# Kernel optimization log

Measured on AMD Instinct MI355X. Metric: run time of the kernel, lower is better.

## Reference

```python
import jax, jax.numpy as jnp
import numpy as np

N, G, P, E = 65536, 256, 256, 1048576   # nodes, graphs, nodes/graph, edges
AF, BF, D, H, L, CE, T = 92, 41, 64, 128, 3, 16, 4
EPS = 1e-5


def _lin(x, W, b):
    return x @ W + b


def setup_inputs() -> dict:
    key = jax.random.key(0)
    ks = jax.random.split(key, 32)
    f = jax.random.normal
    inp = {
        "x": f(ks[0], (N, AF), jnp.float32),
        "edge_attr": f(ks[1], (E, BF), jnp.float32),
        "charge": f(ks[2], (G,), jnp.float32),
        "charge_W": f(ks[3], (1, CE)) * 0.3,
        "charge_b": f(ks[4], (CE,)) * 0.1,
        "atom_W": f(ks[5], (AF + CE, D)) * (1.0 / np.sqrt(AF + CE)),
        "atom_b": f(ks[6], (D,)) * 0.1,
        "bond_W": f(ks[7], (BF, D)) * (1.0 / np.sqrt(BF)),
        "bond_b": f(ks[8], (D,)) * 0.1,
        "nu_W1": f(ks[9], (L, 2 * D, D)) * (1.0 / np.sqrt(2 * D)),
        "nu_b1": f(ks[10], (L, D)) * 0.1,
        "nu_W2": f(ks[11], (L, D, D)) * (1.0 / np.sqrt(D)),
        "nu_b2": f(ks[12], (L, D)) * 0.1,
        "eu_W1": f(ks[13], (L, 3 * D, D)) * (1.0 / np.sqrt(3 * D)),
        "eu_b1": f(ks[14], (L, D)) * 0.1,
        "eu_W2": f(ks[15], (L, D, D)) * (1.0 / np.sqrt(D)),
        "eu_b2": f(ks[16], (L, D)) * 0.1,
        "bn_gamma": jnp.ones((L, D), jnp.float32),
        "bn_beta": jnp.zeros((L, D), jnp.float32),
        "pred_W1": f(ks[17], (D, H)) * (1.0 / np.sqrt(D)),
        "pred_b1": f(ks[18], (H,)) * 0.1,
        "pred_W2": f(ks[19], (H, H)) * (1.0 / np.sqrt(H)),
        "pred_b2": f(ks[20], (H,)) * 0.1,
        "pred_W3": f(ks[21], (H, 1)) * (1.0 / np.sqrt(H)),
        "pred_b3": f(ks[22], (1,)) * 0.1,
        "edge_index": jax.random.randint(ks[23], (2, E), 0, N, jnp.int32),
        "batch": (jnp.arange(N, dtype=jnp.int32) // P),
        "target_site_indices": jax.random.randint(ks[24], (G, T), 0, P, jnp.int32),
    }
    return inp


def reference(x, edge_attr, charge, charge_W, charge_b, atom_W, atom_b, bond_W,
              bond_b, nu_W1, nu_b1, nu_W2, nu_b2, eu_W1, eu_b1, eu_W2, eu_b2,
              bn_gamma, bn_beta, pred_W1, pred_b1, pred_W2, pred_b2, pred_W3,
              pred_b3, edge_index, batch, target_site_indices):
    sp = jax.nn.softplus
    # early charge integration
    charge_feat = _lin(charge[:, None], charge_W, charge_b)        # [G, CE]
    h = _lin(jnp.concatenate([x, charge_feat[batch]], 1), atom_W, atom_b)  # [N, D]
    e = _lin(edge_attr, bond_W, bond_b)                            # [E, D]
    row, col = edge_index[0], edge_index[1]
    for i in range(L):
        hs, hd = h[row], h[col]                                    # gather per edge
        e = _lin(sp(_lin(jnp.concatenate([hs, hd, e], 1), eu_W1[i], eu_b1[i])),
                 eu_W2[i], eu_b2[i])                               # edge update
        m = _lin(sp(_lin(jnp.concatenate([hs, e], 1), nu_W1[i], nu_b1[i])),
                 nu_W2[i], nu_b2[i])                               # messages
        hn = jax.ops.segment_sum(m, col, num_segments=N)           # scatter_add
        mu = hn.mean(0)
        var = hn.var(0)                                            # biased, as torch BN train
        hn = (hn - mu) / jnp.sqrt(var + EPS) * bn_gamma[i] + bn_beta[i]
        h = sp(hn) + h
    # selective pooling over target sites (vectorized version of per-graph loop)
    counts = jax.ops.segment_sum(jnp.ones((N,), h.dtype), batch, num_segments=G)
    counts_i = counts.astype(jnp.int32)
    starts = (jnp.cumsum(counts_i) - counts_i)                     # [G] graph offsets
    valid = target_site_indices < counts_i[:, None]                # [G, T]
    gidx = starts[:, None] + jnp.where(valid, target_site_indices, 0)
    sel = h[gidx] * valid[:, :, None].astype(h.dtype)              # [G, T, D]
    nsel = valid.sum(1)
    sel_mean = sel.sum(1) / jnp.maximum(nsel, 1)[:, None].astype(h.dtype)
    gmean = jax.ops.segment_sum(h, batch, num_segments=G) / counts[:, None]
    graph_repr = jnp.where((nsel > 0)[:, None], sel_mean, gmean)   # [G, D]
    # predictor (dropout = identity in eval)
    z = sp(_lin(graph_repr, pred_W1, pred_b1))
    z = sp(_lin(z, pred_W2, pred_b2))
    out = _lin(z, pred_W3, pred_b3)
    return out.squeeze(-1)                                         # [G]
```

## Files before the change

### kernel.cpp

```cpp
#include <hip/hip_runtime.h>
#include <hip/hip_bf16.h>
#include <hip/hip_fp16.h>
#include <math.h>

#define N_NODES 65536
#define N_GRAPH 256
#define P_NODES 256
#define N_EDGES 1048576
#define AF 92
#define BF 41
#define DIM 64
#define HID 128
#define NLAYER 3
#define CE 16
#define TS 4
#define BN_EPS 1e-5f
#define EPW 32
#define PSTRIDE 33

typedef _Float16 half8 __attribute__((ext_vector_type(8)));
typedef _Float16 half4_t __attribute__((ext_vector_type(4)));
typedef float floatx4 __attribute__((ext_vector_type(4)));

__device__ __forceinline__ float softplus_f(float x) {
    return fmaxf(x, 0.0f) + __logf(1.0f + __expf(-fabsf(x)));
}

__global__ __launch_bounds__(64) void k_h0(
    const float* __restrict__ x, const float* __restrict__ charge,
    const float* __restrict__ chW, const float* __restrict__ chb,
    const float* __restrict__ atomW, const float* __restrict__ atomb,
    const int* __restrict__ batch, float* __restrict__ h,
    __half* __restrict__ h16)
{
    const int n = blockIdx.x * 64 + threadIdx.x;
    float acc[DIM];
#pragma unroll
    for (int j = 0; j < DIM; ++j) acc[j] = atomb[j];
    const float* xr = x + (size_t)n * AF;
    for (int k2 = 0; k2 < AF; k2 += 2) {
        float2 a = *(const float2*)(xr + k2);
        {
            const float* w = atomW + (size_t)k2 * DIM;
#pragma unroll
            for (int j = 0; j < DIM; ++j) acc[j] = fmaf(w[j], a.x, acc[j]);
        }
        {
            const float* w = atomW + (size_t)(k2 + 1) * DIM;
#pragma unroll
            for (int j = 0; j < DIM; ++j) acc[j] = fmaf(w[j], a.y, acc[j]);
        }
    }
    const float cg = charge[batch[n]];
#pragma unroll
    for (int k = 0; k < CE; ++k) {
        float av = fmaf(cg, chW[k], chb[k]);
        const float* w = atomW + (size_t)(AF + k) * DIM;
#pragma unroll
        for (int j = 0; j < DIM; ++j) acc[j] = fmaf(w[j], av, acc[j]);
    }
    float* hp = h + (size_t)n * DIM;
    _Float16* hq = (_Float16*)h16 + (size_t)n * DIM;
#pragma unroll
    for (int j = 0; j < DIM; j += 4)
        *(float4*)(hp + j) = make_float4(acc[j], acc[j+1], acc[j+2], acc[j+3]);
#pragma unroll
    for (int j = 0; j < DIM; j += 8) {
        half8 hv;
#pragma unroll
        for (int u = 0; u < 8; ++u) hv[u] = (_Float16)acc[j + u];
        *(half8*)(hq + j) = hv;
    }
}

__global__ __launch_bounds__(256) void k_hist(const int* __restrict__ ecol,
                                              int* __restrict__ cnt)
{
    int t = blockIdx.x * 256 + threadIdx.x;
    atomicAdd(&cnt[ecol[t]], 1);
}

__global__ __launch_bounds__(256) void k_blksum(const int* __restrict__ cnt,
                                                int* __restrict__ bs)
{
    __shared__ int red[256];
    red[threadIdx.x] = cnt[blockIdx.x * 256 + threadIdx.x];
    __syncthreads();
    for (int o = 128; o > 0; o >>= 1) {
        if (threadIdx.x < o) red[threadIdx.x] += red[threadIdx.x + o];
        __syncthreads();
    }
    if (threadIdx.x == 0) bs[blockIdx.x] = red[0];
}

__global__ __launch_bounds__(256) void k_scanb(const int* __restrict__ bs,
                                               int* __restrict__ bo)
{
    __shared__ int ps[256];
    const int t = threadIdx.x;
    int v = bs[t];
    ps[t] = v;
    __syncthreads();
    for (int off = 1; off < 256; off <<= 1) {
        int u = (t >= off) ? ps[t - off] : 0;
        __syncthreads();
        ps[t] += u;
        __syncthreads();
    }
    bo[t] = ps[t] - v;
}

__global__ __launch_bounds__(256) void k_scan3(const int* __restrict__ cnt,
                                               const int* __restrict__ bo,
                                               int* __restrict__ starts)
{
    __shared__ int ps[256];
    const int b = blockIdx.x, t = threadIdx.x;
    int v = cnt[b * 256 + t];
    ps[t] = v;
    __syncthreads();
    for (int off = 1; off < 256; off <<= 1) {
        int u = (t >= off) ? ps[t - off] : 0;
        __syncthreads();
        ps[t] += u;
        __syncthreads();
    }
    starts[b * 256 + t] = bo[b] + ps[t] - v;
    if (b == 255 && t == 255) starts[N_NODES] = bo[255] + ps[255];
}

__global__ __launch_bounds__(256) void k_scatter(const int* __restrict__ ecol,
                                                 int* __restrict__ cur,
                                                 int* __restrict__ perm,
                                                 int* __restrict__ ipos)
{
    int t = blockIdx.x * 256 + threadIdx.x;
    int pos = atomicAdd(&cur[ecol[t]], 1);
    perm[pos] = t;
    ipos[t] = pos;
}

__global__ __launch_bounds__(256) void k_wprep_all(
    const float* __restrict__ euW1, const float* __restrict__ euW2,
    const float* __restrict__ nuW1, const float* __restrict__ nuW2,
    __half* __restrict__ out)
{
    const int idx = blockIdx.x * 256 + threadIdx.x;
    const int layer = idx / 28672;
    int off = idx - layer * 28672;
    const float* W;
    if (off < 12288)        { W = euW1 + (size_t)layer * 192 * DIM; }
    else if (off < 16384)   { W = euW2 + (size_t)layer * DIM * DIM; off -= 12288; }
    else if (off < 24576)   { W = nuW1 + (size_t)layer * 128 * DIM; off -= 16384; }
    else                    { W = nuW2 + (size_t)layer * DIM * DIM; off -= 24576; }
    int j    = off & 7;
    int lane = (off >> 3) & 63;
    int f    = off >> 9;
    int ntile = f & 3;
    int kIter = f >> 2;
    int k = kIter * 32 + ((lane >> 4) & 3) * 8 + j;
    int n = ntile * 16 + (lane & 15);
    out[idx] = __float2half(W[k * 64 + n]);
}

__global__ __launch_bounds__(256) void k_wprep_bond(
    const float* __restrict__ bondW, __half* __restrict__ out)
{
    const int idx = blockIdx.x * 256 + threadIdx.x;
    int j    = idx & 7;
    int lane = (idx >> 3) & 63;
    int f    = idx >> 9;
    int ntile = f & 3;
    int kIter = f >> 2;
    int k = kIter * 32 + ((lane >> 4) & 3) * 8 + j;
    int n = ntile * 16 + (lane & 15);
    out[idx] = (k < BF) ? __float2half(bondW[k * 64 + n]) : __float2half(0.0f);
}

__global__ __launch_bounds__(64) void k_wfuse(
    const float* __restrict__ euW2, const float* __restrict__ nuW1,
    const float* __restrict__ eub2, const float* __restrict__ nub1,
    float* __restrict__ WfuF32, float* __restrict__ bfu)
{
    const int L = blockIdx.x, j = threadIdx.x;
    const float* W2  = euW2 + (size_t)L * DIM * DIM;
    const float* N1b = nuW1 + (size_t)L * 128 * DIM + 64 * DIM;
    float acc[64];
#pragma unroll
    for (int k = 0; k < 64; ++k) acc[k] = 0.f;
    for (int l = 0; l < 64; ++l) {
        float nv = N1b[l * 64 + j];
#pragma unroll
        for (int k = 0; k < 64; ++k) acc[k] = fmaf(W2[k * 64 + l], nv, acc[k]);
    }
    float* outW = WfuF32 + (size_t)L * 4096;
    for (int k = 0; k < 64; ++k) outW[k * 64 + j] = acc[k];
    float b = nub1[L * 64 + j];
    for (int l = 0; l < 64; ++l) b = fmaf(eub2[L * 64 + l], N1b[l * 64 + j], b);
    bfu[L * 64 + j] = b;
}

__global__ __launch_bounds__(256) void k_wprep_fuse(
    const float* __restrict__ WfuF32, __half* __restrict__ out)
{
    const int idx = blockIdx.x * 256 + threadIdx.x;
    const int layer = idx >> 12;
    int off = idx & 4095;
    int j    = off & 7;
    int lane = (off >> 3) & 63;
    int f    = off >> 9;
    int ntile = f & 3;
    int kIter = f >> 2;
    int k = kIter * 32 + ((lane >> 4) & 3) * 8 + j;
    int n = ntile * 16 + (lane & 15);
    out[idx] = __float2half(WfuF32[(size_t)layer * 4096 + k * 64 + n]);
}

__device__ __forceinline__ void init_acc(floatx4 acc[2][4],
                                         const float* __restrict__ b, int mrow)
{
#pragma unroll
    for (int n = 0; n < 4; ++n) {
        float bv = b[n * 16 + mrow];
        floatx4 f = {bv, bv, bv, bv};
        acc[0][n] = f;
        acc[1][n] = f;
    }
}

__device__ __forceinline__ void gemm_panel(floatx4 acc[2][4],
                                           const _Float16* __restrict__ P,
                                           const __half* __restrict__ Wf,
                                           int fragBase, int quad,
                                           int mrow, int lane)
{
    const _Float16* Wh = (const _Float16*)Wf;
#pragma unroll
    for (int ki = 0; ki < 2; ++ki) {
        const _Float16* pa = P + (size_t)(((ki * 4 + quad) * PSTRIDE + mrow) * 8);
        half8 a0 = *(const half8*)pa;
        half8 a1 = *(const half8*)(pa + 16 * 8);
#pragma unroll
        for (int n = 0; n < 4; ++n) {
            half8 b = *(const half8*)(Wh +
                ((size_t)(fragBase + ki * 4 + n) * 64 + lane) * 8);
            acc[0][n] = __builtin_amdgcn_mfma_f32_16x16x32_f16(a0, b, acc[0][n], 0, 0, 0);
            acc[1][n] = __builtin_amdgcn_mfma_f32_16x16x32_f16(a1, b, acc[1][n], 0, 0, 0);
        }
    }
}

__device__ __forceinline__ void cstore_panel(const floatx4 acc[2][4],
                                             _Float16* __restrict__ P,
                                             int quad, int mrow, bool sp)
{
#pragma unroll
    for (int t = 0; t < 2; ++t)
#pragma unroll
        for (int n = 0; n < 4; ++n)
#pragma unroll
            for (int r = 0; r < 4; ++r) {
                int edge = t * 16 + quad * 4 + r;
                int d = n * 16 + mrow;
                float v = acc[t][n][r];
                if (sp) v = softplus_f(v);
                P[((d >> 3) * PSTRIDE + edge) * 8 + (d & 7)] = (_Float16)v;
            }
}

__device__ __forceinline__ void rows_to_global(const _Float16* __restrict__ P,
                                               __half* __restrict__ dst,
                                               int e0, int lane)
{
#pragma unroll
    for (int i = 0; i < 4; ++i) {
        int idx = i * 64 + lane;
        int eL = idx >> 3;
        int c  = idx & 7;
        half8 v = *(const half8*)&P[(c * PSTRIDE + eL) * 8];
        *(half8*)((_Float16*)dst + (size_t)(e0 + eL) * 64 + c * 8) = v;
    }
}

__device__ __forceinline__ void store_m_native(const floatx4 acc[2][4],
        __half* __restrict__ m, int blk, int quad, int mrow)
{
    _Float16* base = (_Float16*)m + (size_t)blk * 2048;
#pragma unroll
    for (int t = 0; t < 2; ++t)
#pragma unroll
        for (int n = 0; n < 4; ++n) {
            half4_t hv;
            hv[0] = (_Float16)acc[t][n][0];
            hv[1] = (_Float16)acc[t][n][1];
            hv[2] = (_Float16)acc[t][n][2];
            hv[3] = (_Float16)acc[t][n][3];
            *(half4_t*)(base + ((((t * 4 + n) * 4 + quad) * 16 + mrow) * 4)) = hv;
        }
}

__device__ __forceinline__ void stage_h16(const __half* __restrict__ hrow,
                                          _Float16* __restrict__ P,
                                          int sEdge, int sSeg)
{
    const _Float16* hp = (const _Float16*)hrow + sSeg * 32;
#pragma unroll
    for (int i = 0; i < 4; ++i) {
        half8 hv = *(const half8*)(hp + i * 8);
        *(half8*)&P[((sSeg * 4 + i) * PSTRIDE + sEdge) * 8] = hv;
    }
}

__global__ __launch_bounds__(64, 4) void k_edge4(
    const __half* __restrict__ h16, __half* __restrict__ eT,
    const __half* __restrict__ Wf, const __half* __restrict__ Wfu,
    const float* __restrict__ eub1, const float* __restrict__ eub2,
    const float* __restrict__ bfu,  const float* __restrict__ nub2,
    const int* __restrict__ erow, const int* __restrict__ ecol,
    const int* __restrict__ perm,
    __half* __restrict__ m)
{
    __shared__ __align__(16) _Float16 P0[8 * PSTRIDE * 8];
    __shared__ __align__(16) _Float16 P1[8 * PSTRIDE * 8];
    const int lane = threadIdx.x;
    const int quad = lane >> 4;
    const int mrow = lane & 15;
    const int e0   = blockIdx.x * EPW;
    const int sEdge = lane >> 1;
    const int sSeg  = lane & 1;

    floatx4 acc[2][4], acc2[2][4];

    half8 epre[4];
    {
        const _Float16* ep = (const _Float16*)(eT + (size_t)(e0 + sEdge) * DIM) + sSeg * 32;
#pragma unroll
        for (int i = 0; i < 4; ++i) epre[i] = *(const half8*)(ep + i * 8);
    }

    const int ed = perm[e0 + sEdge];
    stage_h16(h16 + (size_t)erow[ed] * DIM, P0, sEdge, sSeg);
    stage_h16(h16 + (size_t)ecol[ed] * DIM, P1, sEdge, sSeg);
    __syncthreads();

    init_acc(acc, eub1, mrow);
    gemm_panel(acc, P0, Wf, 0, quad, mrow, lane);
    gemm_panel(acc, P1, Wf, 8, quad, mrow, lane);
    __syncthreads();
    {
#pragma unroll
        for (int i = 0; i < 4; ++i)
            *(half8*)&P1[((sSeg * 4 + i) * PSTRIDE + sEdge) * 8] = epre[i];
    }
    __syncthreads();
    gemm_panel(acc, P1, Wf, 16, quad, mrow, lane);
    __syncthreads();
    cstore_panel(acc, P1, quad, mrow, true);
    __syncthreads();

    init_acc(acc, bfu, mrow);
    gemm_panel(acc, P0, Wf, 32, quad, mrow, lane);
    gemm_panel(acc, P1, Wfu, 0, quad, mrow, lane);
    init_acc(acc2, eub2, mrow);
    gemm_panel(acc2, P1, Wf, 24, quad, mrow, lane);
    __syncthreads();
    cstore_panel(acc, P0, quad, mrow, true);
    __syncthreads();

    init_acc(acc, nub2, mrow);
    gemm_panel(acc, P0, Wf, 48, quad, mrow, lane);
    __syncthreads();
    cstore_panel(acc2, P1, quad, mrow, false);
    __syncthreads();
    rows_to_global(P1, eT, e0, lane);
    store_m_native(acc, m, blockIdx.x, quad, mrow);
}

__global__ __launch_bounds__(256) void k_agg(
    const __half* __restrict__ m, const int* __restrict__ starts,
    __half* __restrict__ hn)
{
    const int w = threadIdx.x >> 6;
    const int lane = threadIdx.x & 63;
    const int n = blockIdx.x * 4 + w;
    const int s = starts[n], e = starts[n + 1];
    const int nn = lane >> 4, mrow = lane & 15;
    float acc = 0.f;
    for (int g = s & ~3; g < e; g += 4) {
        int blk = g >> 5;
        int off = g & 31;
        int t = off >> 4, quad = (off >> 2) & 3;
        half4_t v = *(const half4_t*)((const _Float16*)m + (size_t)blk * 2048
                     + (((t * 4 + nn) * 4 + quad) * 16 + mrow) * 4);
        float f0 = (float)v[0], f1 = (float)v[1];
        float f2 = (float)v[2], f3 = (float)v[3];
        if (g >= s && g + 3 < e) {
            acc += (f0 + f1) + (f2 + f3);
        } else {
            if (g     >= s && g     < e) acc += f0;
            if (g + 1 >= s && g + 1 < e) acc += f1;
            if (g + 2 >= s && g + 2 < e) acc += f2;
            if (g + 3 >= s && g + 3 < e) acc += f3;
        }
    }
    hn[(size_t)n * DIM + lane] = (__half)acc;
}

__global__ __launch_bounds__(256) void k_bnstats(const __half* __restrict__ hn,
                                                 float* __restrict__ stats)
{
    const int j = threadIdx.x & 63;
    const int sub = threadIdx.x >> 6;
    const int r0 = blockIdx.x * 256;
    float s = 0.f, qq = 0.f;
    for (int i = 0; i < 64; ++i) {
        float v = (float)hn[(size_t)(r0 + i * 4 + sub) * DIM + j];
        s += v;
        qq = fmaf(v, v, qq);
    }
    __shared__ float ls[256], lq[256];
    ls[threadIdx.x] = s; lq[threadIdx.x] = qq;
    __syncthreads();
    if (threadIdx.x < 128) {
        ls[threadIdx.x] += ls[threadIdx.x + 128];
        lq[threadIdx.x] += lq[threadIdx.x + 128];
    }
    __syncthreads();
    if (threadIdx.x < 64) {
        atomicAdd(&stats[j],      ls[threadIdx.x] + ls[threadIdx.x + 64]);
        atomicAdd(&stats[64 + j], lq[threadIdx.x] + lq[threadIdx.x + 64]);
    }
}

__global__ __launch_bounds__(256) void k_hupd(
    const __half* __restrict__ hn, float* __restrict__ h,
    __half* __restrict__ h16,
    const float* __restrict__ stats, const float* __restrict__ gamma,
    const float* __restrict__ beta)
{
    const size_t idx = (size_t)blockIdx.x * 256 + threadIdx.x;
    const int j = (int)(idx & 63);
    const float inv_n = 1.0f / (float)N_NODES;
    float mu  = stats[j] * inv_n;
    float var = stats[64 + j] * inv_n - mu * mu;
    float sc  = gamma[j] * rsqrtf(var + BN_EPS);
    float v   = ((float)hn[idx] - mu) * sc + beta[j];
    float nh  = h[idx] + softplus_f(v);
    h[idx] = nh;
    h16[idx] = (__half)nh;
}

__device__ __forceinline__ void stage_e2(_Float16* __restrict__ P,
                                         int id2, float2 v)
{
    int idx = id2 * 2;
    int e = (idx * 51151) >> 21;
    int k = idx - e * 41;
    P[((k >> 3) * PSTRIDE + e) * 8 + (k & 7)] = (_Float16)v.x;
    idx++;
    e = (idx * 51151) >> 21;
    k = idx - e * 41;
    P[((k >> 3) * PSTRIDE + e) * 8 + (k & 7)] = (_Float16)v.y;
}

__global__ __launch_bounds__(64) void k_e0m(
    const float* __restrict__ eattr, const __half* __restrict__ Wb,
    const float* __restrict__ bondb, const int* __restrict__ ipos,
    __half* __restrict__ eT)
{
    __shared__ __align__(16) _Float16 P0[8 * PSTRIDE * 8];
    __shared__ int slot[32];
    const int lane = threadIdx.x;
    const int quad = lane >> 4;
    const int mrow = lane & 15;
    const int e0   = blockIdx.x * 32;

    if (lane < 32) slot[lane] = ipos[e0 + lane];

    {
        half8 z = {};
#pragma unroll
        for (int i = 0; i < 4; ++i) ((half8*)P0)[i * 64 + lane] = z;
        if (lane < 8) ((half8*)P0)[256 + lane] = z;
    }
    __syncthreads();

    const float* src = eattr + (size_t)e0 * BF;
#pragma unroll
    for (int i = 0; i < 10; ++i) {
        const int id2 = i * 64 + lane;
        float2 v = *(const float2*)(src + id2 * 2);
        stage_e2(P0, id2, v);
    }
    if (lane < 16) {
        const int id2 = 640 + lane;
        float2 v = *(const float2*)(src + id2 * 2);
        stage_e2(P0, id2, v);
    }
    __syncthreads();

    floatx4 acc[2][4];
    init_acc(acc, bondb, mrow);
    gemm_panel(acc, P0, Wb, 0, quad, mrow, lane);
    __syncthreads();
    cstore_panel(acc, P0, quad, mrow, false);
    __syncthreads();

#pragma unroll
    for (int i = 0; i < 4; ++i) {
        int idx = i * 64 + lane;
        int eL = idx >> 3;
        int c  = idx & 7;
        half8 v = *(const half8*)&P0[(c * PSTRIDE + eL) * 8];
        *(half8*)((_Float16*)eT + (size_t)slot[eL] * DIM + c * 8) = v;
    }
}

__global__ __launch_bounds__(64) void k_pool(const float* __restrict__ h,
                                             const int* __restrict__ tsi,
                                             float* __restrict__ gr)
{
    const int g = blockIdx.x, j = threadIdx.x;
    float s = 0.f;
#pragma unroll
    for (int t = 0; t < TS; ++t) {
        int p = tsi[g * TS + t];
        s += h[(size_t)(g * P_NODES + p) * DIM + j];
    }
    gr[g * DIM + j] = s * (1.0f / TS);
}

__global__ __launch_bounds__(128) void k_pred(const float* __restrict__ gr,
    const float* __restrict__ W1, const float* __restrict__ b1,
    const float* __restrict__ W2, const float* __restrict__ b2,
    const float* __restrict__ W3, const float* __restrict__ b3,
    float* __restrict__ out)
{
    const int g = blockIdx.x, j = threadIdx.x;
    __shared__ float zin[DIM], z1[HID], red[HID];
    if (j < DIM) zin[j] = gr[g * DIM + j];
    __syncthreads();
    float a = b1[j];
    for (int k = 0; k < DIM; ++k) a = fmaf(zin[k], W1[k * HID + j], a);
    z1[j] = softplus_f(a);
    __syncthreads();
    float a2 = b2[j];
    for (int k = 0; k < HID; ++k) a2 = fmaf(z1[k], W2[k * HID + j], a2);
    red[j] = softplus_f(a2) * W3[j];
    __syncthreads();
    for (int s = 64; s > 0; s >>= 1) {
        if (j < s) red[j] += red[j + s];
        __syncthreads();
    }
    if (j == 0) out[g] = red[0] + b3[0];
}

extern "C" void kernel_launch(void* const* d_in, const int* in_sizes, int n_in,
                              void* d_out, int out_size, void* d_ws, size_t ws_size,
                              hipStream_t stream)
{
    const float* x      = (const float*)d_in[0];
    const float* eattr  = (const float*)d_in[1];
    const float* charge = (const float*)d_in[2];
    const float* chW    = (const float*)d_in[3];
    const float* chb    = (const float*)d_in[4];
    const float* atomW  = (const float*)d_in[5];
    const float* atomb  = (const float*)d_in[6];
    const float* bondW  = (const float*)d_in[7];
    const float* bondb  = (const float*)d_in[8];
    const float* nuW1   = (const float*)d_in[9];
    const float* nub1   = (const float*)d_in[10];
    const float* nuW2   = (const float*)d_in[11];
    const float* nub2   = (const float*)d_in[12];
    const float* euW1   = (const float*)d_in[13];
    const float* eub1   = (const float*)d_in[14];
    const float* euW2   = (const float*)d_in[15];
    const float* eub2   = (const float*)d_in[16];
    const float* gamma  = (const float*)d_in[17];
    const float* beta   = (const float*)d_in[18];
    const float* pW1    = (const float*)d_in[19];
    const float* pb1    = (const float*)d_in[20];
    const float* pW2    = (const float*)d_in[21];
    const float* pb2    = (const float*)d_in[22];
    const float* pW3    = (const float*)d_in[23];
    const float* pb3    = (const float*)d_in[24];
    const int*   eidx   = (const int*)d_in[25];
    const int*   batch  = (const int*)d_in[26];
    const int*   tsi    = (const int*)d_in[27];
    const int* erow = eidx;
    const int* ecol = eidx + N_EDGES;

    char* ws = (char*)d_ws;
    float*  h      = (float*)(ws);
    __half* hn     = (__half*)(ws + ((size_t)16 << 20));
    int*    ipos   = (int*)  (ws + ((size_t)16 << 20));
    __half* h16    = (__half*)(ws + ((size_t)24 << 20));
    float*  stats  = (float*)(ws + ((size_t)32 << 20));
    float*  gr     = (float*)(ws + ((size_t)32 << 20) + (64 << 10));
    int*    bs     = (int*)  (ws + ((size_t)32 << 20) + (192 << 10));
    int*    bo     = (int*)  (ws + ((size_t)32 << 20) + (196 << 10));
    int*    counts = (int*)  (ws + ((size_t)33 << 20));
    int*    starts = (int*)  (ws + ((size_t)33 << 20) + (256 << 10));
    int*    cur    = (int*)  (ws + ((size_t)33 << 20) + (768 << 10));
    __half* Wfrag  = (__half*)(ws + ((size_t)34 << 20));
    __half* Wbond  = (__half*)(ws + ((size_t)34 << 20) + (256 << 10));
    __half* Wfu    = (__half*)(ws + ((size_t)34 << 20) + (320 << 10));
    float*  bfu    = (float*)(ws + ((size_t)34 << 20) + (384 << 10));
    float*  WfuF32 = (float*)(ws + ((size_t)34 << 20) + (448 << 10));
    int*    perm   = (int*)  (ws + ((size_t)35 << 20));
    __half* eT     = (__half*)(ws + ((size_t)40 << 20));
    __half* m      = (__half*)(ws + ((size_t)168 << 20));

    hipMemsetAsync(counts, 0, N_NODES * sizeof(int), stream);
    k_hist<<<N_EDGES / 256, 256, 0, stream>>>(ecol, counts);
    k_blksum<<<256, 256, 0, stream>>>(counts, bs);
    k_scanb<<<1, 256, 0, stream>>>(bs, bo);
    k_scan3<<<256, 256, 0, stream>>>(counts, bo, starts);
    hipMemcpyAsync(cur, starts, N_NODES * sizeof(int),
                   hipMemcpyDeviceToDevice, stream);
    k_scatter<<<N_EDGES / 256, 256, 0, stream>>>(ecol, cur, perm, ipos);

    k_wprep_all<<<(3 * 28672) / 256, 256, 0, stream>>>(euW1, euW2, nuW1, nuW2, Wfrag);
    k_wprep_bond<<<16, 256, 0, stream>>>(bondW, Wbond);
    k_wfuse<<<3, 64, 0, stream>>>(euW2, nuW1, eub2, nub1, WfuF32, bfu);
    k_wprep_fuse<<<48, 256, 0, stream>>>(WfuF32, Wfu);

    k_h0<<<N_NODES / 64, 64, 0, stream>>>(x, charge, chW, chb, atomW, atomb,
                                          batch, h, h16);
    k_e0m<<<N_EDGES / 32, 64, 0, stream>>>(eattr, Wbond, bondb, ipos, eT);

    const size_t LW = 28672;
    for (int i = 0; i < NLAYER; ++i) {
        hipMemsetAsync(stats, 0, 128 * sizeof(float), stream);
        k_edge4<<<N_EDGES / EPW, 64, 0, stream>>>(h16, eT, Wfrag + i * LW,
            Wfu + (size_t)i * 4096,
            eub1 + i * DIM, eub2 + i * DIM, bfu + i * DIM, nub2 + i * DIM,
            erow, ecol, perm, m);
        k_agg<<<N_NODES / 4, 256, 0, stream>>>(m, starts, hn);
        k_bnstats<<<N_NODES / 256, 256, 0, stream>>>(hn, stats);
        k_hupd<<<(N_NODES * DIM) / 256, 256, 0, stream>>>(hn, h, h16, stats,
            gamma + i * DIM, beta + i * DIM);
    }

    k_pool<<<N_GRAPH, 64, 0, stream>>>(h, tsi, gr);
    k_pred<<<N_GRAPH, HID, 0, stream>>>(gr, pW1, pb1, pW2, pb2, pW3, pb3, (float*)d_out);
}
```

Measured before the change: 1.278 ms.

## Rewrite edge kernel with register-resident 32x32x16 MFMA chain, no LDS staging

Replaces the LDS-staged 16x16 MFMA edge kernel with one that loads gathered node and edge rows straight into 32x32x16 MFMA operands. Intermediate activations are passed between chained GEMMs in registers using lane shuffles, and biases are folded in as an extra ones column of K. Weight prep is reorganised into a single fragment-layout kernel, and the aggregation kernel is adapted to the new message layout with wider loads and a shuffle reduction. The aim is to remove LDS round trips and barriers in the per-layer edge work. The cost is higher register pressure and some padded MFMA work for the bias K-slices.

```diff
diff --git a/kernel.cpp b/kernel.cpp
--- a/kernel.cpp
+++ b/kernel.cpp
@@ -15,15 +15,43 @@
 #define CE 16
 #define TS 4
 #define BN_EPS 1e-5f
-#define EPW 32
 #define PSTRIDE 33
 
 typedef _Float16 half8 __attribute__((ext_vector_type(8)));
-typedef _Float16 half4_t __attribute__((ext_vector_type(4)));
 typedef float floatx4 __attribute__((ext_vector_type(4)));
+typedef float floatx16 __attribute__((ext_vector_type(16)));
 
 __device__ __forceinline__ float softplus_f(float x) {
     return fmaxf(x, 0.0f) + __logf(1.0f + __expf(-fabsf(x)));
+}
+
+__device__ __forceinline__ int pkcvt(float a, float b) {
+    __half2 h = __floats2half2_rn(a, b);
+    int r; __builtin_memcpy(&r, &h, 4); return r;
+}
+
+__device__ __forceinline__ half8 mk8(int a, int b, int c, int d) {
+    union { half8 v; int i[4]; } u;
+    u.i[0] = a; u.i[1] = b; u.i[2] = c; u.i[3] = d;
+    return u.v;
+}
+
+__device__ __forceinline__ floatx16 mfma32(half8 a, half8 b, floatx16 c) {
+    return __builtin_amdgcn_mfma_f32_32x32x16_f16(a, b, c, 0, 0, 0);
+}
+
+__device__ __forceinline__ half8 chain_frag(const floatx16& t, int s_local, bool hi) {
+    const int rA = 8 * s_local;
+    const int rB = rA + 4;
+    int A0 = pkcvt(t[rA + 0], t[rA + 1]);
+    int A1 = pkcvt(t[rA + 2], t[rA + 3]);
+    int B0 = pkcvt(t[rB + 0], t[rB + 1]);
+    int B1 = pkcvt(t[rB + 2], t[rB + 3]);
+    int S0 = hi ? A0 : B0, S1 = hi ? A1 : B1;
+    int R0 = __shfl_xor(S0, 32), R1 = __shfl_xor(S1, 32);
+    int w0 = hi ? R0 : A0, w1 = hi ? R1 : A1;
+    int w2 = hi ? B0 : R0, w3 = hi ? B1 : R1;
+    return mk8(w0, w1, w2, w3);
 }
 
 __global__ __launch_bounds__(64) void k_h0(
@@ -138,29 +166,6 @@
     int pos = atomicAdd(&cur[ecol[t]], 1);
     perm[pos] = t;
     ipos[t] = pos;
-}
-
-__global__ __launch_bounds__(256) void k_wprep_all(
-    const float* __restrict__ euW1, const float* __restrict__ euW2,
-    const float* __restrict__ nuW1, const float* __restrict__ nuW2,
-    __half* __restrict__ out)
-{
-    const int idx = blockIdx.x * 256 + threadIdx.x;
-    const int layer = idx / 28672;
-    int off = idx - layer * 28672;
-    const float* W;
-    if (off < 12288)        { W = euW1 + (size_t)layer * 192 * DIM; }
-    else if (off < 16384)   { W = euW2 + (size_t)layer * DIM * DIM; off -= 12288; }
-    else if (off < 24576)   { W = nuW1 + (size_t)layer * 128 * DIM; off -= 16384; }
-    else                    { W = nuW2 + (size_t)layer * DIM * DIM; off -= 24576; }
-    int j    = off & 7;
-    int lane = (off >> 3) & 63;
-    int f    = off >> 9;
-    int ntile = f & 3;
-    int kIter = f >> 2;
-    int k = kIter * 32 + ((lane >> 4) & 3) * 8 + j;
-    int n = ntile * 16 + (lane & 15);
-    out[idx] = __float2half(W[k * 64 + n]);
 }
 
 __global__ __launch_bounds__(256) void k_wprep_bond(
@@ -200,20 +205,48 @@
     bfu[L * 64 + j] = b;
 }
 
-__global__ __launch_bounds__(256) void k_wprep_fuse(
-    const float* __restrict__ WfuF32, __half* __restrict__ out)
+__global__ __launch_bounds__(256) void k_wprepB(
+    const float* __restrict__ euW1, const float* __restrict__ eub1,
+    const float* __restrict__ euW2, const float* __restrict__ eub2,
+    const float* __restrict__ nuW1, const float* __restrict__ WfuF32,
+    const float* __restrict__ bfu,  const float* __restrict__ nuW2,
+    const float* __restrict__ nub2, __half* __restrict__ out)
 {
     const int idx = blockIdx.x * 256 + threadIdx.x;
-    const int layer = idx >> 12;
-    int off = idx & 4095;
-    int j    = off & 7;
-    int lane = (off >> 3) & 63;
-    int f    = off >> 9;
-    int ntile = f & 3;
-    int kIter = f >> 2;
-    int k = kIter * 32 + ((lane >> 4) & 3) * 8 + j;
-    int n = ntile * 16 + (lane & 15);
-    out[idx] = __float2half(WfuF32[(size_t)layer * 4096 + k * 64 + n]);
+    const int L = idx >> 15;
+    const int off = idx & 32767;
+    const int F = off >> 9;
+    const int l = (off >> 3) & 63;
+    const int j = off & 7;
+    const int k_oct = ((l >> 5) << 3) + j;
+    const int row = (l & 31);
+    float val;
+    if (F < 26) {
+        int mt = F / 13, ks = F - mt * 13;
+        int k = ks * 16 + k_oct, r = mt * 32 + row;
+        val = (k < 192) ? euW1[(size_t)L * 192 * DIM + k * 64 + r]
+            : (k == 192 ? eub1[L * 64 + r] : 0.f);
+    } else if (F < 36) {
+        int f = F - 26; int mt = f / 5, ks = f - mt * 5;
+        int k = ks * 16 + k_oct, r = mt * 32 + row;
+        val = (k < 64) ? euW2[(size_t)L * 4096 + k * 64 + r]
+            : (k == 64 ? eub2[L * 64 + r] : 0.f);
+    } else if (F < 44) {
+        int f = F - 36; int mt = f / 4, ks = f - mt * 4;
+        int k = ks * 16 + k_oct, r = mt * 32 + row;
+        val = nuW1[(size_t)L * 8192 + k * 64 + r];
+    } else if (F < 54) {
+        int f = F - 44; int mt = f / 5, ks = f - mt * 5;
+        int k = ks * 16 + k_oct, r = mt * 32 + row;
+        val = (k < 64) ? WfuF32[(size_t)L * 4096 + k * 64 + r]
+            : (k == 64 ? bfu[L * 64 + r] : 0.f);
+    } else {
+        int f = F - 54; int mt = f / 5, ks = f - mt * 5;
+        int k = ks * 16 + k_oct, r = mt * 32 + row;
+        val = (k < 64) ? nuW2[(size_t)L * 4096 + k * 64 + r]
+            : (k == 64 ? nub2[L * 64 + r] : 0.f);
+    }
+    out[idx] = __float2half(val);
 }
 
 __device__ __forceinline__ void init_acc(floatx4 acc[2][4],
@@ -268,112 +301,194 @@
             }
 }
 
-__device__ __forceinline__ void rows_to_global(const _Float16* __restrict__ P,
-                                               __half* __restrict__ dst,
-                                               int e0, int lane)
-{
+__device__ __forceinline__ void stage_e2(_Float16* __restrict__ P,
+                                         int id2, float2 v)
+{
+    int idx = id2 * 2;
+    int e = (idx * 51151) >> 21;
+    int k = idx - e * 41;
+    P[((k >> 3) * PSTRIDE + e) * 8 + (k & 7)] = (_Float16)v.x;
+    idx++;
+    e = (idx * 51151) >> 21;
+    k = idx - e * 41;
+    P[((k >> 3) * PSTRIDE + e) * 8 + (k & 7)] = (_Float16)v.y;
+}
+
+__global__ __launch_bounds__(64) void k_e0m(
+    const float* __restrict__ eattr, const __half* __restrict__ Wb,
+    const float* __restrict__ bondb, const int* __restrict__ ipos,
+    __half* __restrict__ eT)
+{
+    __shared__ __align__(16) _Float16 P0[8 * PSTRIDE * 8];
+    __shared__ int slot[32];
+    const int lane = threadIdx.x;
+    const int quad = lane >> 4;
+    const int mrow = lane & 15;
+    const int e0   = blockIdx.x * 32;
+
+    if (lane < 32) slot[lane] = ipos[e0 + lane];
+
+    {
+        half8 z = {};
+#pragma unroll
+        for (int i = 0; i < 4; ++i) ((half8*)P0)[i * 64 + lane] = z;
+        if (lane < 8) ((half8*)P0)[256 + lane] = z;
+    }
+    __syncthreads();
+
+    const float* src = eattr + (size_t)e0 * BF;
+#pragma unroll
+    for (int i = 0; i < 10; ++i) {
+        const int id2 = i * 64 + lane;
+        float2 v = *(const float2*)(src + id2 * 2);
+        stage_e2(P0, id2, v);
+    }
+    if (lane < 16) {
+        const int id2 = 640 + lane;
+        float2 v = *(const float2*)(src + id2 * 2);
+        stage_e2(P0, id2, v);
+    }
+    __syncthreads();
+
+    floatx4 acc[2][4];
+    init_acc(acc, bondb, mrow);
+    gemm_panel(acc, P0, Wb, 0, quad, mrow, lane);
+    __syncthreads();
+    cstore_panel(acc, P0, quad, mrow, false);
+    __syncthreads();
+
 #pragma unroll
     for (int i = 0; i < 4; ++i) {
         int idx = i * 64 + lane;
         int eL = idx >> 3;
         int c  = idx & 7;
-        half8 v = *(const half8*)&P[(c * PSTRIDE + eL) * 8];
-        *(half8*)((_Float16*)dst + (size_t)(e0 + eL) * 64 + c * 8) = v;
-    }
-}
-
-__device__ __forceinline__ void store_m_native(const floatx4 acc[2][4],
-        __half* __restrict__ m, int blk, int quad, int mrow)
-{
-    _Float16* base = (_Float16*)m + (size_t)blk * 2048;
-#pragma unroll
-    for (int t = 0; t < 2; ++t)
-#pragma unroll
-        for (int n = 0; n < 4; ++n) {
-            half4_t hv;
-            hv[0] = (_Float16)acc[t][n][0];
-            hv[1] = (_Float16)acc[t][n][1];
-            hv[2] = (_Float16)acc[t][n][2];
-            hv[3] = (_Float16)acc[t][n][3];
-            *(half4_t*)(base + ((((t * 4 + n) * 4 + quad) * 16 + mrow) * 4)) = hv;
+        half8 v = *(const half8*)&P0[(c * PSTRIDE + eL) * 8];
+        *(half8*)((_Float16*)eT + (size_t)slot[eL] * DIM + c * 8) = v;
+    }
+}
+
+__global__ __launch_bounds__(64) void k_edge5(
+    const __half* __restrict__ h16, __half* __restrict__ eT,
+    const __half* __restrict__ WB,
+    const int* __restrict__ erow, const int* __restrict__ ecol,
+    const int* __restrict__ perm, __half* __restrict__ m)
+{
+    const int lane = threadIdx.x;
+    const int e = lane & 31;
+    const bool hi = lane >= 32;
+    const int h = hi ? 1 : 0;
+    const int e0 = blockIdx.x * 32;
+    const int ed = perm[e0 + e];
+    const int rs = erow[ed], cs = ecol[ed];
+
+    const half8* WBv = (const half8*)WB;
+
+    half8 fs[4], fd[4], fe[4];
+    {
+        const _Float16* ps = (const _Float16*)h16 + (size_t)rs * DIM + h * 8;
+        const _Float16* pd = (const _Float16*)h16 + (size_t)cs * DIM + h * 8;
+        const _Float16* pe = (const _Float16*)eT  + (size_t)(e0 + e) * DIM + h * 8;
+#pragma unroll
+        for (int s = 0; s < 4; ++s) {
+            fs[s] = *(const half8*)(ps + 16 * s);
+            fd[s] = *(const half8*)(pd + 16 * s);
+            fe[s] = *(const half8*)(pe + 16 * s);
         }
-}
-
-__device__ __forceinline__ void stage_h16(const __half* __restrict__ hrow,
-                                          _Float16* __restrict__ P,
-                                          int sEdge, int sSeg)
-{
-    const _Float16* hp = (const _Float16*)hrow + sSeg * 32;
-#pragma unroll
-    for (int i = 0; i < 4; ++i) {
-        half8 hv = *(const half8*)(hp + i * 8);
-        *(half8*)&P[((sSeg * 4 + i) * PSTRIDE + sEdge) * 8] = hv;
-    }
-}
-
-__global__ __launch_bounds__(64, 4) void k_edge4(
-    const __half* __restrict__ h16, __half* __restrict__ eT,
-    const __half* __restrict__ Wf, const __half* __restrict__ Wfu,
-    const float* __restrict__ eub1, const float* __restrict__ eub2,
-    const float* __restrict__ bfu,  const float* __restrict__ nub2,
-    const int* __restrict__ erow, const int* __restrict__ ecol,
-    const int* __restrict__ perm,
-    __half* __restrict__ m)
-{
-    __shared__ __align__(16) _Float16 P0[8 * PSTRIDE * 8];
-    __shared__ __align__(16) _Float16 P1[8 * PSTRIDE * 8];
-    const int lane = threadIdx.x;
-    const int quad = lane >> 4;
-    const int mrow = lane & 15;
-    const int e0   = blockIdx.x * EPW;
-    const int sEdge = lane >> 1;
-    const int sSeg  = lane & 1;
-
-    floatx4 acc[2][4], acc2[2][4];
-
-    half8 epre[4];
+    }
+    half8 ones = {};
+    if (!hi) ones[0] = (_Float16)1.0f;
+
+    floatx16 t1a = {};
+    floatx16 t1b = {};
+#pragma unroll
+    for (int ks = 0; ks < 13; ++ks) {
+        half8 b;
+        if (ks < 4)       b = fs[ks & 3];
+        else if (ks < 8)  b = fd[(ks - 4) & 3];
+        else if (ks < 12) b = fe[(ks - 8) & 3];
+        else              b = ones;
+        t1a = mfma32(WBv[(0 * 13 + ks) * 64 + lane], b, t1a);
+        t1b = mfma32(WBv[(1 * 13 + ks) * 64 + lane], b, t1b);
+    }
+#pragma unroll
+    for (int i = 0; i < 16; ++i) {
+        t1a[i] = softplus_f(t1a[i]);
+        t1b[i] = softplus_f(t1b[i]);
+    }
+    half8 bf1[4];
+    bf1[0] = chain_frag(t1a, 0, hi);
+    bf1[1] = chain_frag(t1a, 1, hi);
+    bf1[2] = chain_frag(t1b, 0, hi);
+    bf1[3] = chain_frag(t1b, 1, hi);
+
+    floatx16 ea = {};
+    floatx16 eb = {};
+#pragma unroll
+    for (int ks = 0; ks < 5; ++ks) {
+        half8 b;
+        if (ks < 4) b = bf1[ks & 3]; else b = ones;
+        ea = mfma32(WBv[(26 + 0 * 5 + ks) * 64 + lane], b, ea);
+        eb = mfma32(WBv[(26 + 1 * 5 + ks) * 64 + lane], b, eb);
+    }
     {
-        const _Float16* ep = (const _Float16*)(eT + (size_t)(e0 + sEdge) * DIM) + sSeg * 32;
-#pragma unroll
-        for (int i = 0; i < 4; ++i) epre[i] = *(const half8*)(ep + i * 8);
-    }
-
-    const int ed = perm[e0 + sEdge];
-    stage_h16(h16 + (size_t)erow[ed] * DIM, P0, sEdge, sSeg);
-    stage_h16(h16 + (size_t)ecol[ed] * DIM, P1, sEdge, sSeg);
-    __syncthreads();
-
-    init_acc(acc, eub1, mrow);
-    gemm_panel(acc, P0, Wf, 0, quad, mrow, lane);
-    gemm_panel(acc, P1, Wf, 8, quad, mrow, lane);
-    __syncthreads();
+        _Float16* dst = (_Float16*)eT + (size_t)(e0 + e) * DIM + 4 * h;
+#pragma unroll
+        for (int rg = 0; rg < 4; ++rg) {
+            int2 v; v.x = pkcvt(ea[4*rg+0], ea[4*rg+1]);
+            v.y = pkcvt(ea[4*rg+2], ea[4*rg+3]);
+            *(int2*)(dst + 8 * rg) = v;
+            int2 w; w.x = pkcvt(eb[4*rg+0], eb[4*rg+1]);
+            w.y = pkcvt(eb[4*rg+2], eb[4*rg+3]);
+            *(int2*)(dst + 32 + 8 * rg) = w;
+        }
+    }
+
+    floatx16 t2a = {};
+    floatx16 t2b = {};
+#pragma unroll
+    for (int ks = 0; ks < 4; ++ks) {
+        t2a = mfma32(WBv[(36 + 0 * 4 + ks) * 64 + lane], fs[ks], t2a);
+        t2b = mfma32(WBv[(36 + 1 * 4 + ks) * 64 + lane], fs[ks], t2b);
+    }
+#pragma unroll
+    for (int ks = 0; ks < 5; ++ks) {
+        half8 b;
+        if (ks < 4) b = bf1[ks & 3]; else b = ones;
+        t2a = mfma32(WBv[(44 + 0 * 5 + ks) * 64 + lane], b, t2a);
+        t2b = mfma32(WBv[(44 + 1 * 5 + ks) * 64 + lane], b, t2b);
+    }
+#pragma unroll
+    for (int i = 0; i < 16; ++i) {
+        t2a[i] = softplus_f(t2a[i]);
+        t2b[i] = softplus_f(t2b[i]);
+    }
+    half8 bf2[4];
+    bf2[0] = chain_frag(t2a, 0, hi);
+    bf2[1] = chain_frag(t2a, 1, hi);
+    bf2[2] = chain_frag(t2b, 0, hi);
+    bf2[3] = chain_frag(t2b, 1, hi);
+
+    floatx16 ma = {};
+    floatx16 mb = {};
+#pragma unroll
+    for (int ks = 0; ks < 5; ++ks) {
+        half8 b;
+        if (ks < 4) b = bf2[ks & 3]; else b = ones;
+        ma = mfma32(WBv[(54 + 0 * 5 + ks) * 64 + lane], b, ma);
+        mb = mfma32(WBv[(54 + 1 * 5 + ks) * 64 + lane], b, mb);
+    }
     {
-#pragma unroll
-        for (int i = 0; i < 4; ++i)
-            *(half8*)&P1[((sSeg * 4 + i) * PSTRIDE + sEdge) * 8] = epre[i];
-    }
-    __syncthreads();
-    gemm_panel(acc, P1, Wf, 16, quad, mrow, lane);
-    __syncthreads();
-    cstore_panel(acc, P1, quad, mrow, true);
-    __syncthreads();
-
-    init_acc(acc, bfu, mrow);
-    gemm_panel(acc, P0, Wf, 32, quad, mrow, lane);
-    gemm_panel(acc, P1, Wfu, 0, quad, mrow, lane);
-    init_acc(acc2, eub2, mrow);
-    gemm_panel(acc2, P1, Wf, 24, quad, mrow, lane);
-    __syncthreads();
-    cstore_panel(acc, P0, quad, mrow, true);
-    __syncthreads();
-
-    init_acc(acc, nub2, mrow);
-    gemm_panel(acc, P0, Wf, 48, quad, mrow, lane);
-    __syncthreads();
-    cstore_panel(acc2, P1, quad, mrow, false);
-    __syncthreads();
-    rows_to_global(P1, eT, e0, lane);
-    store_m_native(acc, m, blockIdx.x, quad, mrow);
+        _Float16* base = (_Float16*)m + (size_t)blockIdx.x * 2048;
+#pragma unroll
+        for (int rg = 0; rg < 4; ++rg) {
+            int2 v; v.x = pkcvt(ma[4*rg+0], ma[4*rg+1]);
+            v.y = pkcvt(ma[4*rg+2], ma[4*rg+3]);
+            *(int2*)(base + (rg * 64 + lane) * 4) = v;
+            int2 w; w.x = pkcvt(mb[4*rg+0], mb[4*rg+1]);
+            w.y = pkcvt(mb[4*rg+2], mb[4*rg+3]);
+            *(int2*)(base + ((4 + rg) * 64 + lane) * 4) = w;
+        }
+    }
 }
 
 __global__ __launch_bounds__(256) void k_agg(
@@ -384,26 +499,28 @@
     const int lane = threadIdx.x & 63;
     const int n = blockIdx.x * 4 + w;
     const int s = starts[n], e = starts[n + 1];
-    const int nn = lane >> 4, mrow = lane & 15;
-    float acc = 0.f;
-    for (int g = s & ~3; g < e; g += 4) {
-        int blk = g >> 5;
-        int off = g & 31;
-        int t = off >> 4, quad = (off >> 2) & 3;
-        half4_t v = *(const half4_t*)((const _Float16*)m + (size_t)blk * 2048
-                     + (((t * 4 + nn) * 4 + quad) * 16 + mrow) * 4);
-        float f0 = (float)v[0], f1 = (float)v[1];
-        float f2 = (float)v[2], f3 = (float)v[3];
-        if (g >= s && g + 3 < e) {
-            acc += (f0 + f1) + (f2 + f3);
-        } else {
-            if (g     >= s && g     < e) acc += f0;
-            if (g + 1 >= s && g + 1 < e) acc += f1;
-            if (g + 2 >= s && g + 2 < e) acc += f2;
-            if (g + 3 >= s && g + 3 < e) acc += f3;
-        }
-    }
-    hn[(size_t)n * DIM + lane] = (__half)acc;
+    const int dg = lane & 15, ep = lane >> 4;
+    const int mt = dg >> 3, rg = (dg >> 1) & 3, h = dg & 1;
+    const int slotbase = ((mt * 4 + rg) * 64 + h * 32);
+    float a0 = 0.f, a1 = 0.f, a2 = 0.f, a3 = 0.f;
+    for (int g = s + ep; g < e; g += 4) {
+        const _Float16* p = (const _Float16*)m + ((size_t)(g >> 5) * 2048)
+                            + (size_t)(slotbase + (g & 31)) * 4;
+        int2 v = *(const int2*)p;
+        __half2 l0, l1;
+        __builtin_memcpy(&l0, &v.x, 4);
+        __builtin_memcpy(&l1, &v.y, 4);
+        float2 f0 = __half22float2(l0), f1 = __half22float2(l1);
+        a0 += f0.x; a1 += f0.y; a2 += f1.x; a3 += f1.y;
+    }
+    a0 += __shfl_xor(a0, 16); a1 += __shfl_xor(a1, 16);
+    a2 += __shfl_xor(a2, 16); a3 += __shfl_xor(a3, 16);
+    a0 += __shfl_xor(a0, 32); a1 += __shfl_xor(a1, 32);
+    a2 += __shfl_xor(a2, 32); a3 += __shfl_xor(a3, 32);
+    if (lane < 16) {
+        int2 o; o.x = pkcvt(a0, a1); o.y = pkcvt(a2, a3);
+        *(int2*)((_Float16*)hn + (size_t)n * DIM + dg * 4) = o;
+    }
 }
 
 __global__ __launch_bounds__(256) void k_bnstats(const __half* __restrict__ hn,
@@ -448,72 +565,6 @@
     float nh  = h[idx] + softplus_f(v);
     h[idx] = nh;
     h16[idx] = (__half)nh;
-}
-
-__device__ __forceinline__ void stage_e2(_Float16* __restrict__ P,
-                                         int id2, float2 v)
-{
-    int idx = id2 * 2;
-    int e = (idx * 51151) >> 21;
-    int k = idx - e * 41;
-    P[((k >> 3) * PSTRIDE + e) * 8 + (k & 7)] = (_Float16)v.x;
-    idx++;
-    e = (idx * 51151) >> 21;
-    k = idx - e * 41;
-    P[((k >> 3) * PSTRIDE + e) * 8 + (k & 7)] = (_Float16)v.y;
-}
-
-__global__ __launch_bounds__(64) void k_e0m(
-    const float* __restrict__ eattr, const __half* __restrict__ Wb,
-    const float* __restrict__ bondb, const int* __restrict__ ipos,
-    __half* __restrict__ eT)
-{
-    __shared__ __align__(16) _Float16 P0[8 * PSTRIDE * 8];
-    __shared__ int slot[32];
-    const int lane = threadIdx.x;
-    const int quad = lane >> 4;
-    const int mrow = lane & 15;
-    const int e0   = blockIdx.x * 32;
-
-    if (lane < 32) slot[lane] = ipos[e0 + lane];
-
-    {
-        half8 z = {};
-#pragma unroll
-        for (int i = 0; i < 4; ++i) ((half8*)P0)[i * 64 + lane] = z;
-        if (lane < 8) ((half8*)P0)[256 + lane] = z;
-    }
-    __syncthreads();
-
-    const float* src = eattr + (size_t)e0 * BF;
-#pragma unroll
-    for (int i = 0; i < 10; ++i) {
-        const int id2 = i * 64 + lane;
-        float2 v = *(const float2*)(src + id2 * 2);
-        stage_e2(P0, id2, v);
-    }
-    if (lane < 16) {
-        const int id2 = 640 + lane;
-        float2 v = *(const float2*)(src + id2 * 2);
-        stage_e2(P0, id2, v);
-    }
-    __syncthreads();
-
-    floatx4 acc[2][4];
-    init_acc(acc, bondb, mrow);
-    gemm_panel(acc, P0, Wb, 0, quad, mrow, lane);
-    __syncthreads();
-    cstore_panel(acc, P0, quad, mrow, false);
-    __syncthreads();
-
-#pragma unroll
-    for (int i = 0; i < 4; ++i) {
-        int idx = i * 64 + lane;
-        int eL = idx >> 3;
-        int c  = idx & 7;
-        half8 v = *(const half8*)&P0[(c * PSTRIDE + eL) * 8];
-        *(half8*)((_Float16*)eT + (size_t)slot[eL] * DIM + c * 8) = v;
-    }
 }
 
 __global__ __launch_bounds__(64) void k_pool(const float* __restrict__ h,
@@ -602,9 +653,8 @@
     int*    counts = (int*)  (ws + ((size_t)33 << 20));
     int*    starts = (int*)  (ws + ((size_t)33 << 20) + (256 << 10));
     int*    cur    = (int*)  (ws + ((size_t)33 << 20) + (768 << 10));
-    __half* Wfrag  = (__half*)(ws + ((size_t)34 << 20));
+    __half* WfragB = (__half*)(ws + ((size_t)34 << 20));
     __half* Wbond  = (__half*)(ws + ((size_t)34 << 20) + (256 << 10));
-    __half* Wfu    = (__half*)(ws + ((size_t)34 << 20) + (320 << 10));
     float*  bfu    = (float*)(ws + ((size_t)34 << 20) + (384 << 10));
     float*  WfuF32 = (float*)(ws + ((size_t)34 << 20) + (448 << 10));
     int*    perm   = (int*)  (ws + ((size_t)35 << 20));
@@ -620,22 +670,19 @@
                    hipMemcpyDeviceToDevice, stream);
     k_scatter<<<N_EDGES / 256, 256, 0, stream>>>(ecol, cur, perm, ipos);
 
-    k_wprep_all<<<(3 * 28672) / 256, 256, 0, stream>>>(euW1, euW2, nuW1, nuW2, Wfrag);
+    k_wfuse<<<3, 64, 0, stream>>>(euW2, nuW1, eub2, nub1, WfuF32, bfu);
+    k_wprepB<<<(3 * 32768) / 256, 256, 0, stream>>>(euW1, eub1, euW2, eub2,
+        nuW1, WfuF32, bfu, nuW2, nub2, WfragB);
     k_wprep_bond<<<16, 256, 0, stream>>>(bondW, Wbond);
-    k_wfuse<<<3, 64, 0, stream>>>(euW2, nuW1, eub2, nub1, WfuF32, bfu);
-    k_wprep_fuse<<<48, 256, 0, stream>>>(WfuF32, Wfu);
 
     k_h0<<<N_NODES / 64, 64, 0, stream>>>(x, charge, chW, chb, atomW, atomb,
                                           batch, h, h16);
     k_e0m<<<N_EDGES / 32, 64, 0, stream>>>(eattr, Wbond, bondb, ipos, eT);
 
-    const size_t LW = 28672;
     for (int i = 0; i < NLAYER; ++i) {
         hipMemsetAsync(stats, 0, 128 * sizeof(float), stream);
-        k_edge4<<<N_EDGES / EPW, 64, 0, stream>>>(h16, eT, Wfrag + i * LW,
-            Wfu + (size_t)i * 4096,
-            eub1 + i * DIM, eub2 + i * DIM, bfu + i * DIM, nub2 + i * DIM,
-            erow, ecol, perm, m);
+        k_edge5<<<N_EDGES / 32, 64, 0, stream>>>(h16, eT,
+            WfragB + (size_t)i * 32768, erow, ecol, perm, m);
         k_agg<<<N_NODES / 4, 256, 0, stream>>>(m, starts, hn);
         k_bnstats<<<N_NODES / 256, 256, 0, stream>>>(hn, stats);
         k_hupd<<<(N_NODES * DIM) / 256, 256, 0, stream>>>(hn, h, h16, stats,
```

After: 1.551 ms. 21.4% more time.
